# Optimization experiments

Measured on AMD Instinct MI355X. Metric: run time of the kernel, lower is better.

## Reference

```python
import jax, jax.numpy as jnp
import numpy as np

N = 500000   # total nodes in batched graph
B = 8192     # number of graphs
H = 128      # hidden_dim
L = 3        # num_layer -> feature_dim F = H*L = 384
F = H * L
S2S_STEPS = 3
VOCAB = 143


def setup_inputs() -> dict:
    key = jax.random.key(0)
    ks = jax.random.split(key, 12)
    sc = 0.02
    unit_type = jax.random.randint(ks[0], (N,), 0, VOCAB)
    # sorted segment ids covering every graph (contiguous, all B segments non-empty)
    node2graph = (jnp.arange(N) * B) // N
    return {
        'unit_type': unit_type,
        'node2graph': node2graph,
        'embed':    jax.random.normal(ks[1], (VOCAB, H)) * sc,
        'msg_W1':   jax.random.normal(ks[2], (H, 2 * H)) * sc,
        'msg_b1':   jnp.zeros((H,)),
        'msg_W2':   jax.random.normal(ks[3], (H, H)) * sc,
        'msg_b2':   jnp.zeros((H,)),
        'gru_Wih':  jax.random.normal(ks[4], (3 * H, H)) * sc,
        'gru_Whh':  jax.random.normal(ks[5], (3 * H, H)) * sc,
        'gru_bih':  jnp.zeros((3 * H,)),
        'gru_bhh':  jnp.zeros((3 * H,)),
        'lstm_Wih': jax.random.normal(ks[6], (4 * F, 2 * F)) * sc,
        'lstm_Whh': jax.random.normal(ks[7], (4 * F, F)) * sc,
        'lstm_bih': jnp.zeros((4 * F,)),
        'lstm_bhh': jnp.zeros((4 * F,)),
    }


def _gru_step(x, h, Wih, Whh, bih, bhh):
    # single-timestep PyTorch GRU cell; gate order r, z, n
    gi = x @ Wih.T + bih
    gh = h @ Whh.T + bhh
    ir, iz, inn = jnp.split(gi, 3, axis=-1)
    hr, hz, hn = jnp.split(gh, 3, axis=-1)
    r = jax.nn.sigmoid(ir + hr)
    z = jax.nn.sigmoid(iz + hz)
    n = jnp.tanh(inn + r * hn)
    return (1.0 - z) * n + z * h


def _lstm_step(x, h, c, Wih, Whh, bih, bhh):
    # single-timestep PyTorch LSTM cell; gate order i, f, g, o
    g = x @ Wih.T + bih + h @ Whh.T + bhh
    i, f, gc, o = jnp.split(g, 4, axis=-1)
    c = jax.nn.sigmoid(f) * c + jax.nn.sigmoid(i) * jnp.tanh(gc)
    h = jax.nn.sigmoid(o) * jnp.tanh(c)
    return h, c


def reference(unit_type, node2graph, embed, msg_W1, msg_b1, msg_W2, msg_b2,
              gru_Wih, gru_Whh, gru_bih, gru_bhh,
              lstm_Wih, lstm_Whh, lstm_bih, lstm_bhh):
    # --- node update stack ---
    layer_input = embed[unit_type]          # [N, H]
    hx = layer_input                        # GRU hidden state (1 layer)
    hiddens = []
    for _ in range(L):
        x2 = jnp.concatenate([layer_input, layer_input], axis=-1)   # [N, 2H]
        msg = jnp.maximum(x2 @ msg_W1.T + msg_b1, 0.0) @ msg_W2.T + msg_b2
        hx = _gru_step(msg, hx, gru_Wih, gru_Whh, gru_bih, gru_bhh)
        hiddens.append(hx)
        layer_input = hx
    node_feature = jnp.concatenate(hiddens, axis=-1)                # [N, F]

    # --- Set2Set readout ---
    h = jnp.zeros((B, F), dtype=node_feature.dtype)
    c = jnp.zeros((B, F), dtype=node_feature.dtype)
    q_star = jnp.zeros((B, 2 * F), dtype=node_feature.dtype)
    for _ in range(S2S_STEPS):
        h, c = _lstm_step(q_star, h, c, lstm_Wih, lstm_Whh, lstm_bih, lstm_bhh)
        q = h                                                       # [B, F]
        logits = jnp.sum(q[node2graph] * node_feature, axis=-1)     # [N]
        m = jax.ops.segment_max(logits, node2graph, num_segments=B,
                                indices_are_sorted=True)
        e = jnp.exp(logits - m[node2graph])
        z = jax.ops.segment_sum(e, node2graph, num_segments=B,
                                indices_are_sorted=True)
        att = e / z[node2graph]                                     # [N]
        pooled = jax.ops.segment_sum(att[:, None] * node_feature, node2graph,
                                     num_segments=B, indices_are_sorted=True)
        q_star = jnp.concatenate([q, pooled], axis=-1)              # [B, 2F]

    return q_star, node_feature
```

## Files before the change

### kernel.cpp

```cpp
#include <hip/hip_runtime.h>

typedef unsigned short u16;
typedef unsigned int   u32;
typedef u16 bfx8 __attribute__((ext_vector_type(8)));
typedef __bf16 bf16x8 __attribute__((ext_vector_type(8)));
typedef float  f32x4  __attribute__((ext_vector_type(4)));

#define NH  128
#define NF  384
#define K2F 768
#define NG4 1536

__device__ __forceinline__ float bf2f(u16 u){ return __uint_as_float(((u32)u) << 16); }
__device__ __forceinline__ u16 f2bf(float f){
  u32 x = __float_as_uint(f);
  u32 r = x + 0x7fffu + ((x >> 16) & 1u);
  return (u16)(r >> 16);
}
__device__ __forceinline__ float fsig(float x){ return 1.0f / (1.0f + __expf(-x)); }
__device__ __forceinline__ float ftanh(float x){ return 1.0f - 2.0f / (__expf(2.0f * x) + 1.0f); }

struct P {
  const int *unit_type, *n2g;
  const void *embed, *w1, *b1, *w2, *b2, *gwih, *gwhh, *gbih, *gbhh, *lwih, *lwhh, *lbih, *lbhh;
  int *flag, *segS, *segE;
  u16 *W1eb, *W2b, *Wihb, *Whhb;
  float *b1f, *b2f, *bihG, *bhhG;
  float *Wcat;
  float *bsum;
  float *h1v, *c1v;
  float *hbuf, *cbuf, *pooled;
  float *xcat;
  float *gout;
  u16 *nfb;
  int useNfb;
  void *out; long qsz;
  int N, B, embedN;
};

__device__ __forceinline__ float ldin(const void* p, long i, int isbf){
  return isbf ? bf2f(((const u16*)p)[i]) : ((const float*)p)[i];
}

__global__ void k_detect(P p){
  __shared__ int cnt;
  if (threadIdx.x == 0) cnt = 0;
  __syncthreads();
  const u32* w = (const u32*)p.embed;
  const int nw = p.embedN / 2;
  int bad = 0;
  for (int i = threadIdx.x; i < nw; i += blockDim.x){
    u32 v = w[i];
    float fhi = __uint_as_float(v & 0xffff0000u);
    float flo = __uint_as_float(v << 16);
    if (!(fabsf(fhi) < 2.0f)) bad++;
    if (!(fabsf(flo) < 2.0f)) bad++;
  }
  atomicAdd(&cnt, bad);
  __syncthreads();
  if (threadIdx.x == 0) *p.flag = (cnt == 0) ? 1 : 0;
}

__global__ void k_prep(P p){
  long o = (long)blockIdx.x * 256 + threadIdx.x;
  const int isbf = *p.flag;
  if (o < 16384){ long cc = o >> 7, k = o & 127;
    float v = ldin(p.w1, cc*256 + k, isbf) + ldin(p.w1, cc*256 + 128 + k, isbf);
    p.W1eb[o] = f2bf(v); return; } o -= 16384;
  if (o < 16384){ p.W2b[o]  = f2bf(ldin(p.w2, o, isbf));   return; } o -= 16384;
  if (o < 49152){ p.Wihb[o] = f2bf(ldin(p.gwih, o, isbf)); return; } o -= 49152;
  if (o < 49152){ p.Whhb[o] = f2bf(ldin(p.gwhh, o, isbf)); return; } o -= 49152;
  if (o < (long)NG4*K2F){ long j = o / K2F, k = o - j*K2F;
    float v = ldin(p.lwih, o, isbf);
    if (k < NF) v += ldin(p.lwhh, j*NF + k, isbf);
    p.Wcat[o] = v; return; } o -= (long)NG4*K2F;
  if (o < NH){ p.b1f[o] = ldin(p.b1, o, isbf); return; } o -= NH;
  if (o < NH){ p.b2f[o] = ldin(p.b2, o, isbf); return; } o -= NH;
  if (o < NF){ p.bihG[o] = ldin(p.gbih, o, isbf); return; } o -= NF;
  if (o < NF){ p.bhhG[o] = ldin(p.gbhh, o, isbf); return; } o -= NF;
  if (o < NG4){ p.bsum[o] = ldin(p.lbih, o, isbf) + ldin(p.lbhh, o, isbf); return; } o -= NG4;
  if (o < p.B){ p.segS[o] = 0; p.segE[o] = 0; }
}

__global__ void k_segb(P p){
  int i = (int)blockIdx.x * 256 + threadIdx.x;
  if (i >= p.N) return;
  int g = p.n2g[i];
  if (g < 0 || g >= p.B) return;
  if (i == 0        || p.n2g[i-1] != g) p.segS[g] = i;
  if (i == p.N - 1  || p.n2g[i+1] != g) p.segE[g] = i + 1;
}

__device__ __forceinline__ f32x4 MF(bf16x8 a, bf16x8 b, f32x4 c){
  return __builtin_amdgcn_mfma_f32_16x16x32_bf16(a, b, c, 0, 0, 0);
}
__device__ __forceinline__ bf16x8 ldA(const u16* buf, int m0, int k0, int lane){
  const int row = m0 + (lane & 15);
  const int byte = (row*256 + (k0 + (lane>>4)*8)*2) ^ ((row&7)<<4);
  return *(const bf16x8*)((const char*)buf + byte);
}
__device__ __forceinline__ bf16x8 ldB(const u16* __restrict__ W, int n0, int k0, int lane){
  return *(const bf16x8*)(W + (long)(n0 + (lane&15))*NH + k0 + (lane>>4)*8);
}
__device__ __forceinline__ void stLDS(u16* buf, int row, int col, float v){
  const int byte = (row*256 + col*2) ^ ((row&7)<<4);
  *(u16*)((char*)buf + byte) = f2bf(v);
}
__device__ __forceinline__ float ldLDS(const u16* buf, int row, int col){
  const int byte = (row*256 + col*2) ^ ((row&7)<<4);
  return bf2f(*(const u16*)((const char*)buf + byte));
}
__device__ __forceinline__ u16 ldLDSraw(const u16* buf, int row, int col){
  const int byte = (row*256 + col*2) ^ ((row&7)<<4);
  return *(const u16*)((const char*)buf + byte);
}

__global__ __launch_bounds__(256, 3) void k_stageA_mfma(P p){
  __shared__ u16 hA[64*128];
  __shared__ u16 mA[64*128];
  __shared__ u16 gA[64*128];
  const int t = (int)threadIdx.x;
  const int lane = t & 63, w = t >> 6;
  const int node0 = (int)blockIdx.x * 64;
  const int cL = lane & 15;
  const int isbf = *p.flag;

  {
    const int row = t >> 2, seg = t & 3;
    const int node = min(node0 + row, p.N - 1);
    int ut = p.unit_type[node];
    ut = min(max(ut, 0), p.embedN/NH - 1);
    if (isbf){
      const u16* src = (const u16*)p.embed + (long)ut*NH + seg*32;
      #pragma unroll
      for (int i = 0; i < 4; ++i){
        const int col = seg*32 + i*8;
        const int byte = (row*256 + col*2) ^ ((row&7)<<4);
        *(bfx8*)((char*)hA + byte) = *(const bfx8*)(src + i*8);
      }
    } else {
      const float* src = (const float*)p.embed + (long)ut*NH + seg*32;
      #pragma unroll
      for (int i = 0; i < 4; ++i){
        const int col = seg*32 + i*8;
        u16 tmp[8];
        #pragma unroll
        for (int j = 0; j < 8; ++j) tmp[j] = f2bf(src[i*8 + j]);
        const int byte = (row*256 + col*2) ^ ((row&7)<<4);
        *(bfx8*)((char*)hA + byte) = *(const bfx8*)tmp;
      }
    }
  }
  __syncthreads();

  u16*   out16 = (u16*)p.out;
  float* out32 = (float*)p.out;

  #pragma unroll 1
  for (int l = 0; l < 3; ++l){
    {
      f32x4 acc[2][4];
      #pragma unroll
      for (int nt = 0; nt < 2; ++nt){
        const float b = p.b1f[w*32 + nt*16 + cL];
        #pragma unroll
        for (int m = 0; m < 4; ++m) acc[nt][m] = {b,b,b,b};
      }
      for (int k0 = 0; k0 < 128; k0 += 32){
        bf16x8 a[4];
        #pragma unroll
        for (int m = 0; m < 4; ++m) a[m] = ldA(hA, m*16, k0, lane);
        #pragma unroll
        for (int nt = 0; nt < 2; ++nt){
          const bf16x8 b = ldB(p.W1eb, w*32 + nt*16, k0, lane);
          #pragma unroll
          for (int m = 0; m < 4; ++m) acc[nt][m] = MF(a[m], b, acc[nt][m]);
        }
      }
      #pragma unroll
      for (int nt = 0; nt < 2; ++nt)
        #pragma unroll
        for (int m = 0; m < 4; ++m)
          #pragma unroll
          for (int j = 0; j < 4; ++j)
            stLDS(mA, m*16 + (lane>>4)*4 + j, w*32 + nt*16 + cL,
                  fmaxf(acc[nt][m][j], 0.0f));
    }
    __syncthreads();
    {
      f32x4 acc[2][4];
      #pragma unroll
      for (int nt = 0; nt < 2; ++nt){
        const float b = p.b2f[w*32 + nt*16 + cL];
        #pragma unroll
        for (int m = 0; m < 4; ++m) acc[nt][m] = {b,b,b,b};
      }
      for (int k0 = 0; k0 < 128; k0 += 32){
        bf16x8 a[4];
        #pragma unroll
        for (int m = 0; m < 4; ++m) a[m] = ldA(mA, m*16, k0, lane);
        #pragma unroll
        for (int nt = 0; nt < 2; ++nt){
          const bf16x8 b = ldB(p.W2b, w*32 + nt*16, k0, lane);
          #pragma unroll
          for (int m = 0; m < 4; ++m) acc[nt][m] = MF(a[m], b, acc[nt][m]);
        }
      }
      __syncthreads();
      #pragma unroll
      for (int nt = 0; nt < 2; ++nt)
        #pragma unroll
        for (int m = 0; m < 4; ++m)
          #pragma unroll
          for (int j = 0; j < 4; ++j)
            stLDS(gA, m*16 + (lane>>4)*4 + j, w*32 + nt*16 + cL, acc[nt][m][j]);
    }
    __syncthreads();
    f32x4 rr[2][4];
    {
      f32x4 acc[4][4];
      #pragma unroll
      for (int tc = 0; tc < 4; ++tc){
        const int col = (tc < 2 ? 0 : 128) + w*32 + (tc&1)*16 + cL;
        const float b = p.bihG[col] + p.bhhG[col];
        #pragma unroll
        for (int m = 0; m < 4; ++m) acc[tc][m] = {b,b,b,b};
      }
      for (int k0 = 0; k0 < 128; k0 += 32){
        bf16x8 a[4];
        #pragma unroll
        for (int m = 0; m < 4; ++m) a[m] = ldA(gA, m*16, k0, lane);
        #pragma unroll
        for (int tc = 0; tc < 4; ++tc){
          const bf16x8 b = ldB(p.Wihb, (tc < 2 ? 0 : 128) + w*32 + (tc&1)*16, k0, lane);
          #pragma unroll
          for (int m = 0; m < 4; ++m) acc[tc][m] = MF(a[m], b, acc[tc][m]);
        }
      }
      for (int k0 = 0; k0 < 128; k0 += 32){
        bf16x8 a[4];
        #pragma unroll
        for (int m = 0; m < 4; ++m) a[m] = ldA(hA, m*16, k0, lane);
        #pragma unroll
        for (int tc = 0; tc < 4; ++tc){
          const bf16x8 b = ldB(p.Whhb, (tc < 2 ? 0 : 128) + w*32 + (tc&1)*16, k0, lane);
          #pragma unroll
          for (int m = 0; m < 4; ++m) acc[tc][m] = MF(a[m], b, acc[tc][m]);
        }
      }
      #pragma unroll
      for (int nt = 0; nt < 2; ++nt)
        #pragma unroll
        for (int m = 0; m < 4; ++m)
          #pragma unroll
          for (int j = 0; j < 4; ++j){
            rr[nt][m][j] = fsig(acc[nt][m][j]);
            stLDS(mA, m*16 + (lane>>4)*4 + j, w*32 + nt*16 + cL,
                  fsig(acc[nt+2][m][j]));
          }
    }
    {
      f32x4 inn[2][4], hnn[2][4];
      #pragma unroll
      for (int nt = 0; nt < 2; ++nt){
        const int col = 256 + w*32 + nt*16 + cL;
        const float bi = p.bihG[col], bh = p.bhhG[col];
        #pragma unroll
        for (int m = 0; m < 4; ++m){ inn[nt][m] = {bi,bi,bi,bi}; hnn[nt][m] = {bh,bh,bh,bh}; }
      }
      for (int k0 = 0; k0 < 128; k0 += 32){
        bf16x8 a[4];
        #pragma unroll
        for (int m = 0; m < 4; ++m) a[m] = ldA(gA, m*16, k0, lane);
        #pragma unroll
        for (int nt = 0; nt < 2; ++nt){
          const bf16x8 b = ldB(p.Wihb, 256 + w*32 + nt*16, k0, lane);
          #pragma unroll
          for (int m = 0; m < 4; ++m) inn[nt][m] = MF(a[m], b, inn[nt][m]);
        }
      }
      for (int k0 = 0; k0 < 128; k0 += 32){
        bf16x8 a[4];
        #pragma unroll
        for (int m = 0; m < 4; ++m) a[m] = ldA(hA, m*16, k0, lane);
        #pragma unroll
        for (int nt = 0; nt < 2; ++nt){
          const bf16x8 b = ldB(p.Whhb, 256 + w*32 + nt*16, k0, lane);
          #pragma unroll
          for (int m = 0; m < 4; ++m) hnn[nt][m] = MF(a[m], b, hnn[nt][m]);
        }
      }
      #pragma unroll
      for (int nt = 0; nt < 2; ++nt)
        #pragma unroll
        for (int m = 0; m < 4; ++m)
          #pragma unroll
          for (int j = 0; j < 4; ++j){
            const int row = m*16 + (lane>>4)*4 + j;
            const int col = w*32 + nt*16 + cL;
            const float nn = ftanh(fmaf(rr[nt][m][j], hnn[nt][m][j], inn[nt][m][j]));
            const float zv = ldLDS(mA, row, col);
            const float hv = ldLDS(hA, row, col);
            inn[nt][m][j] = fmaf(zv, hv - nn, nn);
          }
      __syncthreads();
      #pragma unroll
      for (int nt = 0; nt < 2; ++nt)
        #pragma unroll
        for (int m = 0; m < 4; ++m)
          #pragma unroll
          for (int j = 0; j < 4; ++j)
            stLDS(hA, m*16 + (lane>>4)*4 + j, w*32 + nt*16 + cL, inn[nt][m][j]);
      __syncthreads();
    }
    {
      const int col = t & 127;
      const int rh  = t >> 7;
      #pragma unroll 4
      for (int rb = 0; rb < 64; rb += 2){
        const int row = rb + rh;
        const int node = node0 + row;
        if (node < p.N){
          const u16 hv16 = ldLDSraw(hA, row, col);
          const long fi = (long)node*NF + l*NH + col;
          if (isbf){
            __builtin_nontemporal_store(hv16, &out16[p.qsz + fi]);
          } else {
            __builtin_nontemporal_store(bf2f(hv16), &out32[p.qsz + fi]);
            if (p.useNfb) __builtin_nontemporal_store(hv16, &p.nfb[fi]);
          }
        }
      }
    }
  }
}

__global__ void k_lstm0(P p){
  const int d = (int)threadIdx.x;
  if (d >= NF) return;
  const float i_ = fsig(p.bsum[d]);
  const float gc = ftanh(p.bsum[2*NF + d]);
  const float o_ = fsig(p.bsum[3*NF + d]);
  const float cn = i_ * gc;
  p.c1v[d] = cn;
  p.h1v[d] = o_ * ftanh(cn);
}

__global__ __launch_bounds__(256) void k_attn(P p, const float* __restrict__ qsrc,
                                              int qstride, int finalstep){
  __shared__ alignas(16) char raw[32 * NF * 4];
  __shared__ float qs[NF];
  __shared__ float att[32];
  __shared__ float sM, sZ, sSc;

  u16*   nb = (u16*)raw;
  float* nfl = (float*)raw;
  const int t = (int)threadIdx.x;
  const int g = (int)blockIdx.x;
  const int isbf = *p.flag;
  const int bftile = isbf | p.useNfb;
  const u16* nbase = isbf ? (const u16*)p.out + p.qsz : p.nfb;
  const float* o32 = (const float*)p.out;

  for (int i = t; i < NF; i += 256) qs[i] = qsrc[(long)g*qstride + i];
  if (t == 0){ sM = -1e30f; sZ = 0.0f; sSc = 1.0f; }
  int n0 = p.segS[g], n1 = p.segE[g];
  n0 = max(n0, 0); n1 = min(n1, p.N);
  float acc0 = 0.f, acc1 = 0.f;
  __syncthreads();

  for (int base = n0; base < n1; base += 32){
    const int cnt = min(32, n1 - base);
    {
      const int i = t >> 3, q8 = t & 7;
      if (i < cnt){
        if (bftile){
          const bfx8* src = (const bfx8*)(nbase + (long)(base + i)*NF + q8*48);
          #pragma unroll
          for (int j8 = 0; j8 < 6; ++j8)
            *(bfx8*)&nb[i*NF + q8*48 + j8*8] = __builtin_nontemporal_load(src + j8);
        } else {
          const f32x4* src = (const f32x4*)(o32 + p.qsz + (long)(base + i)*NF + q8*48);
          #pragma unroll
          for (int j4 = 0; j4 < 12; ++j4)
            *(f32x4*)&nfl[i*NF + q8*48 + j4*4] = __builtin_nontemporal_load(src + j4);
        }
      }
    }
    __syncthreads();
    {
      const int w = t >> 6, lane = t & 63;
      for (int ii = w; ii < cnt; ii += 4){
        float dot = 0.f;
        #pragma unroll
        for (int j = 0; j < 6; ++j){
          const int d = lane + 64*j;
          const float v = bftile ? bf2f(nb[ii*NF + d]) : nfl[ii*NF + d];
          dot = fmaf(v, qs[d], dot);
        }
        #pragma unroll
        for (int off = 32; off; off >>= 1) dot += __shfl_xor(dot, off);
        if (lane == 0) att[ii] = dot;
      }
    }
    __syncthreads();
    if (t < 32){
      const float l = (t < cnt) ? att[t] : -1e30f;
      float m = l;
      #pragma unroll
      for (int off = 16; off; off >>= 1) m = fmaxf(m, __shfl_xor(m, off));
      const float mnew = fmaxf(sM, m);
      const float e = (t < cnt) ? __expf(l - mnew) : 0.f;
      float z = e;
      #pragma unroll
      for (int off = 16; off; off >>= 1) z += __shfl_xor(z, off);
      if (t < cnt) att[t] = e;
      if (t == 0){
        const float sc = __expf(sM - mnew);
        sSc = sc; sZ = sZ * sc + z; sM = mnew;
      }
    }
    __syncthreads();
    {
      const float sc = sSc;
      acc0 *= sc; acc1 *= sc;
      for (int ii = 0; ii < cnt; ++ii){
        const float a = att[ii];
        const float v0 = bftile ? bf2f(nb[ii*NF + t]) : nfl[ii*NF + t];
        acc0 = fmaf(a, v0, acc0);
        if (t < 128){
          const float v1 = bftile ? bf2f(nb[ii*NF + 256 + t]) : nfl[ii*NF + 256 + t];
          acc1 = fmaf(a, v1, acc1);
        }
      }
    }
    __syncthreads();
  }

  const float invZ = (sZ != 0.0f) ? 1.0f / sZ : 0.0f;
  const float p0 = acc0 * invZ, p1 = acc1 * invZ;
  p.pooled[(long)g*NF + t] = p0;
  if (t < 128) p.pooled[(long)g*NF + 256 + t] = p1;
  if (finalstep){
    const long rb = (long)g * K2F;
    if (isbf){
      u16* o = (u16*)p.out;
      o[rb + t] = f2bf(qs[t]);
      if (t < 128) o[rb + 256 + t] = f2bf(qs[256 + t]);
      o[rb + NF + t] = f2bf(p0);
      if (t < 128) o[rb + NF + 256 + t] = f2bf(p1);
    } else {
      float* o = (float*)p.out;
      o[rb + t] = qs[t];
      if (t < 128) o[rb + 256 + t] = qs[256 + t];
      o[rb + NF + t] = p0;
      if (t < 128) o[rb + NF + 256 + t] = p1;
    }
  }
}

__global__ void k_xcat(P p, const float* __restrict__ hsrc, int hstride){
  const int d2 = (int)blockIdx.x * 256 + threadIdx.x;
  const int g  = (int)blockIdx.y;
  if (d2 >= K2F) return;
  const float v = (d2 < NF) ? hsrc[(long)g*hstride + d2]
                            : p.pooled[(long)g*NF + d2 - NF];
  p.xcat[(long)g*K2F + d2] = v;
}

__global__ __launch_bounds__(256) void k_gemm(P p){
  __shared__ alignas(16) float aT[32][128];
  __shared__ alignas(16) float wT[32][128];
  const int t = (int)threadIdx.x;
  const int tx = t & 15, ty = t >> 4;
  const int row0 = (int)blockIdx.x * 128, col0 = (int)blockIdx.y * 128;
  const int M = p.B;
  float acc[8][8];
  #pragma unroll
  for (int i = 0; i < 8; ++i)
    #pragma unroll
    for (int j = 0; j < 8; ++j) acc[i][j] = 0.f;

  const int r = t >> 1, ks = (t & 1) * 16;
  for (int kc = 0; kc < K2F; kc += 32){
    {
      const int gr = row0 + r;
      float v[16];
      if (gr < M){
        const float* src = p.xcat + (long)gr*K2F + kc + ks;
        *(float4*)&v[0]  = *(const float4*)(src);
        *(float4*)&v[4]  = *(const float4*)(src + 4);
        *(float4*)&v[8]  = *(const float4*)(src + 8);
        *(float4*)&v[12] = *(const float4*)(src + 12);
      } else {
        #pragma unroll
        for (int j = 0; j < 16; ++j) v[j] = 0.f;
      }
      #pragma unroll
      for (int j = 0; j < 16; ++j) aT[ks+j][r] = v[j];
      const float* wsrc = p.Wcat + (long)(col0 + r)*K2F + kc + ks;
      *(float4*)&v[0]  = *(const float4*)(wsrc);
      *(float4*)&v[4]  = *(const float4*)(wsrc + 4);
      *(float4*)&v[8]  = *(const float4*)(wsrc + 8);
      *(float4*)&v[12] = *(const float4*)(wsrc + 12);
      #pragma unroll
      for (int j = 0; j < 16; ++j) wT[ks+j][r] = v[j];
    }
    __syncthreads();
    #pragma unroll 2
    for (int k = 0; k < 32; ++k){
      float a[8], wv[8];
      *(float4*)&a[0]  = *(const float4*)&aT[k][ty*8];
      *(float4*)&a[4]  = *(const float4*)&aT[k][ty*8 + 4];
      *(float4*)&wv[0] = *(const float4*)&wT[k][tx*8];
      *(float4*)&wv[4] = *(const float4*)&wT[k][tx*8 + 4];
      #pragma unroll
      for (int i = 0; i < 8; ++i)
        #pragma unroll
        for (int j = 0; j < 8; ++j) acc[i][j] = fmaf(a[i], wv[j], acc[i][j]);
    }
    __syncthreads();
  }
  float bs[8];
  #pragma unroll
  for (int j = 0; j < 8; ++j) bs[j] = p.bsum[col0 + tx*8 + j];
  #pragma unroll
  for (int i = 0; i < 8; ++i){
    const int gr = row0 + ty*8 + i;
    if (gr < M){
      float* crow = p.gout + (long)gr*NG4 + col0 + tx*8;
      float o[8];
      #pragma unroll
      for (int j = 0; j < 8; ++j) o[j] = acc[i][j] + bs[j];
      *(float4*)&crow[0] = *(const float4*)&o[0];
      *(float4*)&crow[4] = *(const float4*)&o[4];
    }
  }
}

__global__ void k_gates(P p, const float* __restrict__ csrc, int cstride){
  const long idx = (long)blockIdx.x * 256 + threadIdx.x;
  if (idx >= (long)p.B * NF) return;
  const int g = (int)(idx / NF), d = (int)(idx - (long)g*NF);
  const float* gr = p.gout + (long)g*NG4;
  const float i_ = fsig(gr[d]);
  const float f_ = fsig(gr[NF + d]);
  const float gc = ftanh(gr[2*NF + d]);
  const float o_ = fsig(gr[3*NF + d]);
  const float cp = csrc[(long)g*cstride + d];
  const float cn = fmaf(f_, cp, i_ * gc);
  p.cbuf[(long)g*NF + d] = cn;
  p.hbuf[(long)g*NF + d] = o_ * ftanh(cn);
}

extern "C" void kernel_launch(void* const* d_in, const int* in_sizes, int n_in,
                              void* d_out, int out_size, void* d_ws, size_t ws_size,
                              hipStream_t stream){
  P p{};
  p.unit_type = (const int*)d_in[0];
  p.n2g  = (const int*)d_in[1];
  p.embed = d_in[2];  p.w1 = d_in[3];  p.b1 = d_in[4];  p.w2 = d_in[5];  p.b2 = d_in[6];
  p.gwih = d_in[7];  p.gwhh = d_in[8]; p.gbih = d_in[9]; p.gbhh = d_in[10];
  p.lwih = d_in[11]; p.lwhh = d_in[12]; p.lbih = d_in[13]; p.lbhh = d_in[14];

  const int N = in_sizes[0];
  const int B = (int)(((long)out_size - (long)N*NF) / K2F);
  p.N = N; p.B = B; p.embedN = in_sizes[2];
  p.out = d_out; p.qsz = (long)B * K2F;

  char* w = (char*)d_ws;
  size_t used = 0;
  auto alloc = [&](size_t bytes) -> char* {
    char* r = w + used;
    used += (bytes + 255) & ~(size_t)255;
    return r;
  };
  p.flag  = (int*)alloc(4);
  p.segS  = (int*)alloc((size_t)B*4);
  p.segE  = (int*)alloc((size_t)B*4);
  p.W1eb  = (u16*)  alloc(16384*2);
  p.W2b   = (u16*)  alloc(16384*2);
  p.Wihb  = (u16*)  alloc(49152*2);
  p.Whhb  = (u16*)  alloc(49152*2);
  p.b1f   = (float*)alloc(NH*4);
  p.b2f   = (float*)alloc(NH*4);
  p.bihG  = (float*)alloc(NF*4);
  p.bhhG  = (float*)alloc(NF*4);
  p.Wcat  = (float*)alloc((size_t)NG4*K2F*4);
  p.bsum  = (float*)alloc(NG4*4);
  p.h1v   = (float*)alloc(NF*4);
  p.c1v   = (float*)alloc(NF*4);
  p.hbuf  = (float*)alloc((size_t)B*NF*4);
  p.cbuf  = (float*)alloc((size_t)B*NF*4);
  p.pooled= (float*)alloc((size_t)B*NF*4);
  p.xcat  = (float*)alloc((size_t)B*K2F*4);
  p.gout  = (float*)alloc((size_t)B*NG4*4);
  if (used > ws_size){
    (void)hipMemsetAsync(d_out, 0, (size_t)out_size * 2, stream);
    return;
  }
  const size_t nfbBytes = (size_t)N * NF * 2;
  if (used + nfbBytes + 256 <= ws_size){
    p.nfb = (u16*)alloc(nfbBytes);
    p.useNfb = 1;
  } else {
    p.nfb = (u16*)p.flag;
    p.useNfb = 0;
  }

  const long prepTot = 16384 + 16384 + 49152 + 49152
                     + (long)NG4*K2F + NH + NH + NF + NF + NG4 + B;

  k_detect<<<1, 256, 0, stream>>>(p);
  k_prep  <<<(int)((prepTot + 255)/256), 256, 0, stream>>>(p);
  k_segb  <<<(N + 255)/256, 256, 0, stream>>>(p);
  k_stageA_mfma<<<(N + 63)/64, 256, 0, stream>>>(p);
  k_lstm0 <<<1, NF, 0, stream>>>(p);

  const int gemmGx = (B + 127)/128;
  k_attn <<<B, 256, 0, stream>>>(p, p.h1v, 0, 0);
  k_xcat <<<dim3(3, B), 256, 0, stream>>>(p, p.h1v, 0);
  k_gemm <<<dim3(gemmGx, NG4/128), 256, 0, stream>>>(p);
  k_gates<<<(int)(((long)B*NF + 255)/256), 256, 0, stream>>>(p, p.c1v, 0);
  k_attn <<<B, 256, 0, stream>>>(p, p.hbuf, NF, 0);
  k_xcat <<<dim3(3, B), 256, 0, stream>>>(p, p.hbuf, NF);
  k_gemm <<<dim3(gemmGx, NG4/128), 256, 0, stream>>>(p);
  k_gates<<<(int)(((long)B*NF + 255)/256), 256, 0, stream>>>(p, p.cbuf, NF);
  k_attn <<<B, 256, 0, stream>>>(p, p.hbuf, NF, 1);
}
```

Baseline: 2.265 ms.

## Defer node-feature stores to one vectorized write of all three layers

```diff
diff --git a/kernel.cpp b/kernel.cpp
--- a/kernel.cpp
+++ b/kernel.cpp
@@ -106,13 +106,17 @@
   const int byte = (row*256 + col*2) ^ ((row&7)<<4);
   *(u16*)((char*)buf + byte) = f2bf(v);
 }
+__device__ __forceinline__ void stLDSu(u16* buf, int row, int col, u16 v){
+  const int byte = (row*256 + col*2) ^ ((row&7)<<4);
+  *(u16*)((char*)buf + byte) = v;
+}
 __device__ __forceinline__ float ldLDS(const u16* buf, int row, int col){
   const int byte = (row*256 + col*2) ^ ((row&7)<<4);
   return bf2f(*(const u16*)((const char*)buf + byte));
 }
-__device__ __forceinline__ u16 ldLDSraw(const u16* buf, int row, int col){
-  const int byte = (row*256 + col*2) ^ ((row&7)<<4);
-  return *(const u16*)((const char*)buf + byte);
+__device__ __forceinline__ bfx8 ldLDS8(const u16* buf, int row, int col8){
+  const int byte = (row*256 + col8*2) ^ ((row&7)<<4);
+  return *(const bfx8*)((const char*)buf + byte);
 }
 
 __global__ __launch_bounds__(256, 3) void k_stageA_mfma(P p){
@@ -125,6 +129,8 @@
   const int cL = lane & 15;
   const int isbf = *p.flag;
 
+  u16 st[2][2][4][4];
+
   {
     const int row = t >> 2, seg = t & 3;
     const int node = min(node0 + row, p.N - 1);
@@ -309,25 +315,59 @@
         #pragma unroll
         for (int m = 0; m < 4; ++m)
           #pragma unroll
-          for (int j = 0; j < 4; ++j)
-            stLDS(hA, m*16 + (lane>>4)*4 + j, w*32 + nt*16 + cL, inn[nt][m][j]);
+          for (int j = 0; j < 4; ++j){
+            const u16 hv16 = f2bf(inn[nt][m][j]);
+            stLDSu(hA, m*16 + (lane>>4)*4 + j, w*32 + nt*16 + cL, hv16);
+            if (l == 0) st[0][nt][m][j] = hv16;
+            else if (l == 1) st[1][nt][m][j] = hv16;
+          }
       __syncthreads();
     }
-    {
-      const int col = t & 127;
-      const int rh  = t >> 7;
-      #pragma unroll 4
-      for (int rb = 0; rb < 64; rb += 2){
-        const int row = rb + rh;
-        const int node = node0 + row;
-        if (node < p.N){
-          const u16 hv16 = ldLDSraw(hA, row, col);
-          const long fi = (long)node*NF + l*NH + col;
-          if (isbf){
-            __builtin_nontemporal_store(hv16, &out16[p.qsz + fi]);
-          } else {
-            __builtin_nontemporal_store(bf2f(hv16), &out32[p.qsz + fi]);
-            if (p.useNfb) __builtin_nontemporal_store(hv16, &p.nfb[fi]);
+  }
+
+  #pragma unroll
+  for (int nt = 0; nt < 2; ++nt)
+    #pragma unroll
+    for (int m = 0; m < 4; ++m)
+      #pragma unroll
+      for (int j = 0; j < 4; ++j){
+        const int row = m*16 + (lane>>4)*4 + j;
+        const int col = w*32 + nt*16 + cL;
+        stLDSu(mA, row, col, st[0][nt][m][j]);
+        stLDSu(gA, row, col, st[1][nt][m][j]);
+      }
+  __syncthreads();
+
+  {
+    const int r0 = t >> 4;
+    const int c8 = (t & 15) * 8;
+    #pragma unroll
+    for (int r4 = 0; r4 < 4; ++r4){
+      const int row = r0 + r4*16;
+      const int node = node0 + row;
+      if (node < p.N){
+        const bfx8 v0 = ldLDS8(mA, row, c8);
+        const bfx8 v1 = ldLDS8(gA, row, c8);
+        const bfx8 v2 = ldLDS8(hA, row, c8);
+        const long base = (long)node*NF;
+        if (isbf){
+          __builtin_nontemporal_store(v0, (bfx8*)(out16 + p.qsz + base + c8));
+          __builtin_nontemporal_store(v1, (bfx8*)(out16 + p.qsz + base + NH + c8));
+          __builtin_nontemporal_store(v2, (bfx8*)(out16 + p.qsz + base + 2*NH + c8));
+        } else {
+          #pragma unroll
+          for (int lyr = 0; lyr < 3; ++lyr){
+            const bfx8 v = lyr == 0 ? v0 : (lyr == 1 ? v1 : v2);
+            f32x4 lo, hi;
+            #pragma unroll
+            for (int j = 0; j < 4; ++j){ lo[j] = bf2f(v[j]); hi[j] = bf2f(v[j+4]); }
+            __builtin_nontemporal_store(lo, (f32x4*)(out32 + p.qsz + base + lyr*NH + c8));
+            __builtin_nontemporal_store(hi, (f32x4*)(out32 + p.qsz + base + lyr*NH + c8 + 4));
+          }
+          if (p.useNfb){
+            __builtin_nontemporal_store(v0, (bfx8*)(p.nfb + base + c8));
+            __builtin_nontemporal_store(v1, (bfx8*)(p.nfb + base + NH + c8));
+            __builtin_nontemporal_store(v2, (bfx8*)(p.nfb + base + 2*NH + c8));
           }
         }
       }
```

Result: slower. 2.373 ms (+4.7%).

## Move LSTM gate GEMM to bf16 MFMA and persist stage-A tiles

Applied to the files above, without the earlier changes.

```diff
diff --git a/kernel.cpp b/kernel.cpp
--- a/kernel.cpp
+++ b/kernel.cpp
@@ -24,13 +24,14 @@
   const int *unit_type, *n2g;
   const void *embed, *w1, *b1, *w2, *b2, *gwih, *gwhh, *gbih, *gbhh, *lwih, *lwhh, *lbih, *lbhh;
   int *flag, *segS, *segE;
+  u16 *embedB;
   u16 *W1eb, *W2b, *Wihb, *Whhb;
   float *b1f, *b2f, *bihG, *bhhG;
-  float *Wcat;
+  u16 *WcatB;
   float *bsum;
   float *h1v, *c1v;
   float *hbuf, *cbuf, *pooled;
-  float *xcat;
+  u16 *xcatB;
   float *gout;
   u16 *nfb;
   int useNfb;
@@ -64,6 +65,7 @@
 __global__ void k_prep(P p){
   long o = (long)blockIdx.x * 256 + threadIdx.x;
   const int isbf = *p.flag;
+  if (o < p.embedN){ p.embedB[o] = f2bf(ldin(p.embed, o, isbf)); return; } o -= p.embedN;
   if (o < 16384){ long cc = o >> 7, k = o & 127;
     float v = ldin(p.w1, cc*256 + k, isbf) + ldin(p.w1, cc*256 + 128 + k, isbf);
     p.W1eb[o] = f2bf(v); return; } o -= 16384;
@@ -73,7 +75,7 @@
   if (o < (long)NG4*K2F){ long j = o / K2F, k = o - j*K2F;
     float v = ldin(p.lwih, o, isbf);
     if (k < NF) v += ldin(p.lwhh, j*NF + k, isbf);
-    p.Wcat[o] = v; return; } o -= (long)NG4*K2F;
+    p.WcatB[o] = f2bf(v); return; } o -= (long)NG4*K2F;
   if (o < NH){ p.b1f[o] = ldin(p.b1, o, isbf); return; } o -= NH;
   if (o < NH){ p.b2f[o] = ldin(p.b2, o, isbf); return; } o -= NH;
   if (o < NF){ p.bihG[o] = ldin(p.gbih, o, isbf); return; } o -= NF;
@@ -102,6 +104,10 @@
 __device__ __forceinline__ bf16x8 ldB(const u16* __restrict__ W, int n0, int k0, int lane){
   return *(const bf16x8*)(W + (long)(n0 + (lane&15))*NH + k0 + (lane>>4)*8);
 }
+__device__ __forceinline__ bf16x8 ldBs(const u16* __restrict__ W, long stride,
+                                       int n0, int k0, int lane){
+  return *(const bf16x8*)(W + (long)(n0 + (lane&15))*stride + k0 + (lane>>4)*8);
+}
 __device__ __forceinline__ void stLDS(u16* buf, int row, int col, float v){
   const int byte = (row*256 + col*2) ^ ((row&7)<<4);
   *(u16*)((char*)buf + byte) = f2bf(v);
@@ -121,213 +127,205 @@
   __shared__ u16 gA[64*128];
   const int t = (int)threadIdx.x;
   const int lane = t & 63, w = t >> 6;
-  const int node0 = (int)blockIdx.x * 64;
   const int cL = lane & 15;
   const int isbf = *p.flag;
-
-  {
-    const int row = t >> 2, seg = t & 3;
-    const int node = min(node0 + row, p.N - 1);
-    int ut = p.unit_type[node];
-    ut = min(max(ut, 0), p.embedN/NH - 1);
-    if (isbf){
-      const u16* src = (const u16*)p.embed + (long)ut*NH + seg*32;
+  const int nTiles = (p.N + 63) >> 6;
+
+  u16*   out16 = (u16*)p.out;
+  float* out32 = (float*)p.out;
+
+  for (int tile = (int)blockIdx.x; tile < nTiles; tile += (int)gridDim.x){
+    const int node0 = tile * 64;
+    __syncthreads();
+
+    {
+      const int row = t >> 2, seg = t & 3;
+      const int node = min(node0 + row, p.N - 1);
+      int ut = p.unit_type[node];
+      ut = min(max(ut, 0), p.embedN/NH - 1);
+      const u16* src = p.embedB + (long)ut*NH + seg*32;
       #pragma unroll
       for (int i = 0; i < 4; ++i){
         const int col = seg*32 + i*8;
         const int byte = (row*256 + col*2) ^ ((row&7)<<4);
         *(bfx8*)((char*)hA + byte) = *(const bfx8*)(src + i*8);
       }
-    } else {
-      const float* src = (const float*)p.embed + (long)ut*NH + seg*32;
-      #pragma unroll
-      for (int i = 0; i < 4; ++i){
-        const int col = seg*32 + i*8;
-        u16 tmp[8];
-        #pragma unroll
-        for (int j = 0; j < 8; ++j) tmp[j] = f2bf(src[i*8 + j]);
-        const int byte = (row*256 + col*2) ^ ((row&7)<<4);
-        *(bfx8*)((char*)hA + byte) = *(const bfx8*)tmp;
-      }
-    }
-  }
-  __syncthreads();
-
-  u16*   out16 = (u16*)p.out;
-  float* out32 = (float*)p.out;
-
-  #pragma unroll 1
-  for (int l = 0; l < 3; ++l){
-    {
-      f32x4 acc[2][4];
-      #pragma unroll
-      for (int nt = 0; nt < 2; ++nt){
-        const float b = p.b1f[w*32 + nt*16 + cL];
-        #pragma unroll
-        for (int m = 0; m < 4; ++m) acc[nt][m] = {b,b,b,b};
-      }
-      for (int k0 = 0; k0 < 128; k0 += 32){
-        bf16x8 a[4];
-        #pragma unroll
-        for (int m = 0; m < 4; ++m) a[m] = ldA(hA, m*16, k0, lane);
+    }
+    __syncthreads();
+
+    #pragma unroll 1
+    for (int l = 0; l < 3; ++l){
+      {
+        f32x4 acc[2][4];
         #pragma unroll
         for (int nt = 0; nt < 2; ++nt){
-          const bf16x8 b = ldB(p.W1eb, w*32 + nt*16, k0, lane);
-          #pragma unroll
-          for (int m = 0; m < 4; ++m) acc[nt][m] = MF(a[m], b, acc[nt][m]);
-        }
-      }
-      #pragma unroll
-      for (int nt = 0; nt < 2; ++nt)
-        #pragma unroll
-        for (int m = 0; m < 4; ++m)
-          #pragma unroll
-          for (int j = 0; j < 4; ++j)
-            stLDS(mA, m*16 + (lane>>4)*4 + j, w*32 + nt*16 + cL,
-                  fmaxf(acc[nt][m][j], 0.0f));
-    }
-    __syncthreads();
-    {
-      f32x4 acc[2][4];
-      #pragma unroll
-      for (int nt = 0; nt < 2; ++nt){
-        const float b = p.b2f[w*32 + nt*16 + cL];
-        #pragma unroll
-        for (int m = 0; m < 4; ++m) acc[nt][m] = {b,b,b,b};
-      }
-      for (int k0 = 0; k0 < 128; k0 += 32){
-        bf16x8 a[4];
-        #pragma unroll
-        for (int m = 0; m < 4; ++m) a[m] = ldA(mA, m*16, k0, lane);
+          const float b = p.b1f[w*32 + nt*16 + cL];
+          #pragma unroll
+          for (int m = 0; m < 4; ++m) acc[nt][m] = {b,b,b,b};
+        }
+        for (int k0 = 0; k0 < 128; k0 += 32){
+          bf16x8 a[4];
+          #pragma unroll
+          for (int m = 0; m < 4; ++m) a[m] = ldA(hA, m*16, k0, lane);
+          #pragma unroll
+          for (int nt = 0; nt < 2; ++nt){
+            const bf16x8 b = ldB(p.W1eb, w*32 + nt*16, k0, lane);
+            #pragma unroll
+            for (int m = 0; m < 4; ++m) acc[nt][m] = MF(a[m], b, acc[nt][m]);
+          }
+        }
+        #pragma unroll
+        for (int nt = 0; nt < 2; ++nt)
+          #pragma unroll
+          for (int m = 0; m < 4; ++m)
+            #pragma unroll
+            for (int j = 0; j < 4; ++j)
+              stLDS(mA, m*16 + (lane>>4)*4 + j, w*32 + nt*16 + cL,
+                    fmaxf(acc[nt][m][j], 0.0f));
+      }
+      __syncthreads();
+      {
+        f32x4 acc[2][4];
         #pragma unroll
         for (int nt = 0; nt < 2; ++nt){
-          const bf16x8 b = ldB(p.W2b, w*32 + nt*16, k0, lane);
-          #pragma unroll
-          for (int m = 0; m < 4; ++m) acc[nt][m] = MF(a[m], b, acc[nt][m]);
-        }
+          const float b = p.b2f[w*32 + nt*16 + cL];
+          #pragma unroll
+          for (int m = 0; m < 4; ++m) acc[nt][m] = {b,b,b,b};
+        }
+        for (int k0 = 0; k0 < 128; k0 += 32){
+          bf16x8 a[4];
+          #pragma unroll
+          for (int m = 0; m < 4; ++m) a[m] = ldA(mA, m*16, k0, lane);
+          #pragma unroll
+          for (int nt = 0; nt < 2; ++nt){
+            const bf16x8 b = ldB(p.W2b, w*32 + nt*16, k0, lane);
+            #pragma unroll
+            for (int m = 0; m < 4; ++m) acc[nt][m] = MF(a[m], b, acc[nt][m]);
+          }
+        }
+        __syncthreads();
+        #pragma unroll
+        for (int nt = 0; nt < 2; ++nt)
+          #pragma unroll
+          for (int m = 0; m < 4; ++m)
+            #pragma unroll
+            for (int j = 0; j < 4; ++j)
+              stLDS(gA, m*16 + (lane>>4)*4 + j, w*32 + nt*16 + cL, acc[nt][m][j]);
       }
       __syncthreads();
-      #pragma unroll
-      for (int nt = 0; nt < 2; ++nt)
-        #pragma unroll
-        for (int m = 0; m < 4; ++m)
-          #pragma unroll
-          for (int j = 0; j < 4; ++j)
-            stLDS(gA, m*16 + (lane>>4)*4 + j, w*32 + nt*16 + cL, acc[nt][m][j]);
-    }
-    __syncthreads();
-    f32x4 rr[2][4];
-    {
-      f32x4 acc[4][4];
-      #pragma unroll
-      for (int tc = 0; tc < 4; ++tc){
-        const int col = (tc < 2 ? 0 : 128) + w*32 + (tc&1)*16 + cL;
-        const float b = p.bihG[col] + p.bhhG[col];
-        #pragma unroll
-        for (int m = 0; m < 4; ++m) acc[tc][m] = {b,b,b,b};
-      }
-      for (int k0 = 0; k0 < 128; k0 += 32){
-        bf16x8 a[4];
-        #pragma unroll
-        for (int m = 0; m < 4; ++m) a[m] = ldA(gA, m*16, k0, lane);
+      f32x4 rr[2][4];
+      {
+        f32x4 acc[4][4];
         #pragma unroll
         for (int tc = 0; tc < 4; ++tc){
-          const bf16x8 b = ldB(p.Wihb, (tc < 2 ? 0 : 128) + w*32 + (tc&1)*16, k0, lane);
-          #pragma unroll
-          for (int m = 0; m < 4; ++m) acc[tc][m] = MF(a[m], b, acc[tc][m]);
-        }
-      }
-      for (int k0 = 0; k0 < 128; k0 += 32){
-        bf16x8 a[4];
-        #pragma unroll
-        for (int m = 0; m < 4; ++m) a[m] = ldA(hA, m*16, k0, lane);
-        #pragma unroll
-        for (int tc = 0; tc < 4; ++tc){
-          const bf16x8 b = ldB(p.Whhb, (tc < 2 ? 0 : 128) + w*32 + (tc&1)*16, k0, lane);
-          #pragma unroll
-          for (int m = 0; m < 4; ++m) acc[tc][m] = MF(a[m], b, acc[tc][m]);
-        }
-      }
-      #pragma unroll
-      for (int nt = 0; nt < 2; ++nt)
-        #pragma unroll
-        for (int m = 0; m < 4; ++m)
-          #pragma unroll
-          for (int j = 0; j < 4; ++j){
-            rr[nt][m][j] = fsig(acc[nt][m][j]);
-            stLDS(mA, m*16 + (lane>>4)*4 + j, w*32 + nt*16 + cL,
-                  fsig(acc[nt+2][m][j]));
+          const int col = (tc < 2 ? 0 : 128) + w*32 + (tc&1)*16 + cL;
+          const float b = p.bihG[col] + p.bhhG[col];
+          #pragma unroll
+          for (int m = 0; m < 4; ++m) acc[tc][m] = {b,b,b,b};
+        }
+        for (int k0 = 0; k0 < 128; k0 += 32){
+          bf16x8 a[4];
+          #pragma unroll
+          for (int m = 0; m < 4; ++m) a[m] = ldA(gA, m*16, k0, lane);
+          #pragma unroll
+          for (int tc = 0; tc < 4; ++tc){
+            const bf16x8 b = ldB(p.Wihb, (tc < 2 ? 0 : 128) + w*32 + (tc&1)*16, k0, lane);
+            #pragma unroll
+            for (int m = 0; m < 4; ++m) acc[tc][m] = MF(a[m], b, acc[tc][m]);
           }
-    }
-    {
-      f32x4 inn[2][4], hnn[2][4];
-      #pragma unroll
-      for (int nt = 0; nt < 2; ++nt){
-        const int col = 256 + w*32 + nt*16 + cL;
-        const float bi = p.bihG[col], bh = p.bhhG[col];
-        #pragma unroll
-        for (int m = 0; m < 4; ++m){ inn[nt][m] = {bi,bi,bi,bi}; hnn[nt][m] = {bh,bh,bh,bh}; }
-      }
-      for (int k0 = 0; k0 < 128; k0 += 32){
-        bf16x8 a[4];
-        #pragma unroll
-        for (int m = 0; m < 4; ++m) a[m] = ldA(gA, m*16, k0, lane);
+        }
+        for (int k0 = 0; k0 < 128; k0 += 32){
+          bf16x8 a[4];
+          #pragma unroll
+          for (int m = 0; m < 4; ++m) a[m] = ldA(hA, m*16, k0, lane);
+          #pragma unroll
+          for (int tc = 0; tc < 4; ++tc){
+            const bf16x8 b = ldB(p.Whhb, (tc < 2 ? 0 : 128) + w*32 + (tc&1)*16, k0, lane);
+            #pragma unroll
+            for (int m = 0; m < 4; ++m) acc[tc][m] = MF(a[m], b, acc[tc][m]);
+          }
+        }
+        #pragma unroll
+        for (int nt = 0; nt < 2; ++nt)
+          #pragma unroll
+          for (int m = 0; m < 4; ++m)
+            #pragma unroll
+            for (int j = 0; j < 4; ++j){
+              rr[nt][m][j] = fsig(acc[nt][m][j]);
+              stLDS(mA, m*16 + (lane>>4)*4 + j, w*32 + nt*16 + cL,
+                    fsig(acc[nt+2][m][j]));
+            }
+      }
+      {
+        f32x4 inn[2][4], hnn[2][4];
         #pragma unroll
         for (int nt = 0; nt < 2; ++nt){
-          const bf16x8 b = ldB(p.Wihb, 256 + w*32 + nt*16, k0, lane);
-          #pragma unroll
-          for (int m = 0; m < 4; ++m) inn[nt][m] = MF(a[m], b, inn[nt][m]);
-        }
-      }
-      for (int k0 = 0; k0 < 128; k0 += 32){
-        bf16x8 a[4];
-        #pragma unroll
-        for (int m = 0; m < 4; ++m) a[m] = ldA(hA, m*16, k0, lane);
-        #pragma unroll
-        for (int nt = 0; nt < 2; ++nt){
-          const bf16x8 b = ldB(p.Whhb, 256 + w*32 + nt*16, k0, lane);
-          #pragma unroll
-          for (int m = 0; m < 4; ++m) hnn[nt][m] = MF(a[m], b, hnn[nt][m]);
-        }
-      }
-      #pragma unroll
-      for (int nt = 0; nt < 2; ++nt)
-        #pragma unroll
-        for (int m = 0; m < 4; ++m)
-          #pragma unroll
-          for (int j = 0; j < 4; ++j){
-            const int row = m*16 + (lane>>4)*4 + j;
-            const int col = w*32 + nt*16 + cL;
-            const float nn = ftanh(fmaf(rr[nt][m][j], hnn[nt][m][j], inn[nt][m][j]));
-            const float zv = ldLDS(mA, row, col);
-            const float hv = ldLDS(hA, row, col);
-            inn[nt][m][j] = fmaf(zv, hv - nn, nn);
+          const int col = 256 + w*32 + nt*16 + cL;
+          const float bi = p.bihG[col], bh = p.bhhG[col];
+          #pragma unroll
+          for (int m = 0; m < 4; ++m){ inn[nt][m] = {bi,bi,bi,bi}; hnn[nt][m] = {bh,bh,bh,bh}; }
+        }
+        for (int k0 = 0; k0 < 128; k0 += 32){
+          bf16x8 a[4];
+          #pragma unroll
+          for (int m = 0; m < 4; ++m) a[m] = ldA(gA, m*16, k0, lane);
+          #pragma unroll
+          for (int nt = 0; nt < 2; ++nt){
+            const bf16x8 b = ldB(p.Wihb, 256 + w*32 + nt*16, k0, lane);
+            #pragma unroll
+            for (int m = 0; m < 4; ++m) inn[nt][m] = MF(a[m], b, inn[nt][m]);
           }
-      __syncthreads();
-      #pragma unroll
-      for (int nt = 0; nt < 2; ++nt)
-        #pragma unroll
-        for (int m = 0; m < 4; ++m)
-          #pragma unroll
-          for (int j = 0; j < 4; ++j)
-            stLDS(hA, m*16 + (lane>>4)*4 + j, w*32 + nt*16 + cL, inn[nt][m][j]);
-      __syncthreads();
-    }
-    {
-      const int col = t & 127;
-      const int rh  = t >> 7;
-      #pragma unroll 4
-      for (int rb = 0; rb < 64; rb += 2){
-        const int row = rb + rh;
-        const int node = node0 + row;
-        if (node < p.N){
-          const u16 hv16 = ldLDSraw(hA, row, col);
-          const long fi = (long)node*NF + l*NH + col;
-          if (isbf){
-            __builtin_nontemporal_store(hv16, &out16[p.qsz + fi]);
-          } else {
-            __builtin_nontemporal_store(bf2f(hv16), &out32[p.qsz + fi]);
-            if (p.useNfb) __builtin_nontemporal_store(hv16, &p.nfb[fi]);
+        }
+        for (int k0 = 0; k0 < 128; k0 += 32){
+          bf16x8 a[4];
+          #pragma unroll
+          for (int m = 0; m < 4; ++m) a[m] = ldA(hA, m*16, k0, lane);
+          #pragma unroll
+          for (int nt = 0; nt < 2; ++nt){
+            const bf16x8 b = ldB(p.Whhb, 256 + w*32 + nt*16, k0, lane);
+            #pragma unroll
+            for (int m = 0; m < 4; ++m) hnn[nt][m] = MF(a[m], b, hnn[nt][m]);
+          }
+        }
+        #pragma unroll
+        for (int nt = 0; nt < 2; ++nt)
+          #pragma unroll
+          for (int m = 0; m < 4; ++m)
+            #pragma unroll
+            for (int j = 0; j < 4; ++j){
+              const int row = m*16 + (lane>>4)*4 + j;
+              const int col = w*32 + nt*16 + cL;
+              const float nn = ftanh(fmaf(rr[nt][m][j], hnn[nt][m][j], inn[nt][m][j]));
+              const float zv = ldLDS(mA, row, col);
+              const float hv = ldLDS(hA, row, col);
+              inn[nt][m][j] = fmaf(zv, hv - nn, nn);
+            }
+        __syncthreads();
+        #pragma unroll
+        for (int nt = 0; nt < 2; ++nt)
+          #pragma unroll
+          for (int m = 0; m < 4; ++m)
+            #pragma unroll
+            for (int j = 0; j < 4; ++j)
+              stLDS(hA, m*16 + (lane>>4)*4 + j, w*32 + nt*16 + cL, inn[nt][m][j]);
+        __syncthreads();
+      }
+      {
+        const int col = t & 127;
+        const int rh  = t >> 7;
+        #pragma unroll 4
+        for (int rb = 0; rb < 64; rb += 2){
+          const int row = rb + rh;
+          const int node = node0 + row;
+          if (node < p.N){
+            const u16 hv16 = ldLDSraw(hA, row, col);
+            const long fi = (long)node*NF + l*NH + col;
+            if (isbf){
+              __builtin_nontemporal_store(hv16, &out16[p.qsz + fi]);
+            } else {
+              __builtin_nontemporal_store(bf2f(hv16), &out32[p.qsz + fi]);
+              if (p.useNfb) __builtin_nontemporal_store(hv16, &p.nfb[fi]);
+            }
           }
         }
       }
@@ -465,76 +463,60 @@
   if (d2 >= K2F) return;
   const float v = (d2 < NF) ? hsrc[(long)g*hstride + d2]
                             : p.pooled[(long)g*NF + d2 - NF];
-  p.xcat[(long)g*K2F + d2] = v;
-}
-
-__global__ __launch_bounds__(256) void k_gemm(P p){
-  __shared__ alignas(16) float aT[32][128];
-  __shared__ alignas(16) float wT[32][128];
+  p.xcatB[(long)g*K2F + d2] = f2bf(v);
+}
+
+__global__ __launch_bounds__(256, 4) void k_gemm_mfma(P p){
+  __shared__ u16 aT[64*128];
   const int t = (int)threadIdx.x;
-  const int tx = t & 15, ty = t >> 4;
-  const int row0 = (int)blockIdx.x * 128, col0 = (int)blockIdx.y * 128;
-  const int M = p.B;
-  float acc[8][8];
+  const int lane = t & 63, w = t >> 6, cL = lane & 15;
+  const int row0 = (int)blockIdx.x * 64, col0 = (int)blockIdx.y * 128;
+
+  f32x4 acc[2][4];
   #pragma unroll
-  for (int i = 0; i < 8; ++i)
+  for (int nt = 0; nt < 2; ++nt)
     #pragma unroll
-    for (int j = 0; j < 8; ++j) acc[i][j] = 0.f;
-
-  const int r = t >> 1, ks = (t & 1) * 16;
-  for (int kc = 0; kc < K2F; kc += 32){
+    for (int m = 0; m < 4; ++m) acc[nt][m] = {0.f,0.f,0.f,0.f};
+
+  for (int kc = 0; kc < K2F; kc += 128){
+    __syncthreads();
     {
-      const int gr = row0 + r;
-      float v[16];
-      if (gr < M){
-        const float* src = p.xcat + (long)gr*K2F + kc + ks;
-        *(float4*)&v[0]  = *(const float4*)(src);
-        *(float4*)&v[4]  = *(const float4*)(src + 4);
-        *(float4*)&v[8]  = *(const float4*)(src + 8);
-        *(float4*)&v[12] = *(const float4*)(src + 12);
-      } else {
-        #pragma unroll
-        for (int j = 0; j < 16; ++j) v[j] = 0.f;
-      }
+      const int row = t >> 2, seg = t & 3;
+      const int gr = row0 + row;
+      const u16* src = p.xcatB + (long)gr*K2F + kc + seg*32;
       #pragma unroll
-      for (int j = 0; j < 16; ++j) aT[ks+j][r] = v[j];
-      const float* wsrc = p.Wcat + (long)(col0 + r)*K2F + kc + ks;
-      *(float4*)&v[0]  = *(const float4*)(wsrc);
-      *(float4*)&v[4]  = *(const float4*)(wsrc + 4);
-      *(float4*)&v[8]  = *(const float4*)(wsrc + 8);
-      *(float4*)&v[12] = *(const float4*)(wsrc + 12);
+      for (int i = 0; i < 4; ++i){
+        const int col = seg*32 + i*8;
+        const int byte = (row*256 + col*2) ^ ((row&7)<<4);
+        bfx8 v = {0,0,0,0,0,0,0,0};
+        if (gr < p.B) v = *(const bfx8*)(src + i*8);
+        *(bfx8*)((char*)aT + byte) = v;
+      }
+    }
+    __syncthreads();
+    for (int k0 = 0; k0 < 128; k0 += 32){
+      bf16x8 a[4];
       #pragma unroll
-      for (int j = 0; j < 16; ++j) wT[ks+j][r] = v[j];
-    }
-    __syncthreads();
-    #pragma unroll 2
-    for (int k = 0; k < 32; ++k){
-      float a[8], wv[8];
-      *(float4*)&a[0]  = *(const float4*)&aT[k][ty*8];
-      *(float4*)&a[4]  = *(const float4*)&aT[k][ty*8 + 4];
-      *(float4*)&wv[0] = *(const float4*)&wT[k][tx*8];
-      *(float4*)&wv[4] = *(const float4*)&wT[k][tx*8 + 4];
+      for (int m = 0; m < 4; ++m) a[m] = ldA(aT, m*16, k0, lane);
       #pragma unroll
-      for (int i = 0; i < 8; ++i)
-        #pragma unroll
-        for (int j = 0; j < 8; ++j) acc[i][j] = fmaf(a[i], wv[j], acc[i][j]);
-    }
-    __syncthreads();
-  }
-  float bs[8];
+      for (int nt = 0; nt < 2; ++nt){
+        const bf16x8 b = ldBs(p.WcatB, K2F, col0 + w*32 + nt*16, kc + k0, lane);
+        #pragma unroll
+        for (int m = 0; m < 4; ++m) acc[nt][m] = MF(a[m], b, acc[nt][m]);
+      }
+    }
+  }
   #pragma unroll
-  for (int j = 0; j < 8; ++j) bs[j] = p.bsum[col0 + tx*8 + j];
-  #pragma unroll
-  for (int i = 0; i < 8; ++i){
-    const int gr = row0 + ty*8 + i;
-    if (gr < M){
-      float* crow = p.gout + (long)gr*NG4 + col0 + tx*8;
-      float o[8];
+  for (int nt = 0; nt < 2; ++nt){
+    const int col = col0 + w*32 + nt*16 + cL;
+    const float bs = p.bsum[col];
+    #pragma unroll
+    for (int m = 0; m < 4; ++m)
       #pragma unroll
-      for (int j = 0; j < 8; ++j) o[j] = acc[i][j] + bs[j];
-      *(float4*)&crow[0] = *(const float4*)&o[0];
-      *(float4*)&crow[4] = *(const float4*)&o[4];
-    }
+      for (int j = 0; j < 4; ++j){
+        const int row = row0 + m*16 + (lane>>4)*4 + j;
+        if (row < p.B) p.gout[(long)row*NG4 + col] = acc[nt][m][j] + bs;
+      }
   }
 }
 
@@ -578,6 +560,7 @@
   p.flag  = (int*)alloc(4);
   p.segS  = (int*)alloc((size_t)B*4);
   p.segE  = (int*)alloc((size_t)B*4);
+  p.embedB= (u16*)  alloc((size_t)p.embedN*2);
   p.W1eb  = (u16*)  alloc(16384*2);
   p.W2b   = (u16*)  alloc(16384*2);
   p.Wihb  = (u16*)  alloc(49152*2);
@@ -586,14 +569,14 @@
   p.b2f   = (float*)alloc(NH*4);
   p.bihG  = (float*)alloc(NF*4);
   p.bhhG  = (float*)alloc(NF*4);
-  p.Wcat  = (float*)alloc((size_t)NG4*K2F*4);
+  p.WcatB = (u16*)  alloc((size_t)NG4*K2F*2);
   p.bsum  = (float*)alloc(NG4*4);
   p.h1v   = (float*)alloc(NF*4);
   p.c1v   = (float*)alloc(NF*4);
   p.hbuf  = (float*)alloc((size_t)B*NF*4);
   p.cbuf  = (float*)alloc((size_t)B*NF*4);
   p.pooled= (float*)alloc((size_t)B*NF*4);
-  p.xcat  = (float*)alloc((size_t)B*K2F*4);
+  p.xcatB = (u16*)  alloc((size_t)B*K2F*2);
   p.gout  = (float*)alloc((size_t)B*NG4*4);
   if (used > ws_size){
     (void)hipMemsetAsync(d_out, 0, (size_t)out_size * 2, stream);
@@ -608,23 +591,24 @@
     p.useNfb = 0;
   }
 
-  const long prepTot = 16384 + 16384 + 49152 + 49152
+  const long prepTot = (long)p.embedN + 16384 + 16384 + 49152 + 49152
                      + (long)NG4*K2F + NH + NH + NF + NF + NG4 + B;
 
   k_detect<<<1, 256, 0, stream>>>(p);
   k_prep  <<<(int)((prepTot + 255)/256), 256, 0, stream>>>(p);
   k_segb  <<<(N + 255)/256, 256, 0, stream>>>(p);
-  k_stageA_mfma<<<(N + 63)/64, 256, 0, stream>>>(p);
+  const int saGrid = min((N + 63)/64, 2048);
+  k_stageA_mfma<<<saGrid, 256, 0, stream>>>(p);
   k_lstm0 <<<1, NF, 0, stream>>>(p);
 
-  const int gemmGx = (B + 127)/128;
+  const dim3 gemmG((B + 63)/64, NG4/128);
   k_attn <<<B, 256, 0, stream>>>(p, p.h1v, 0, 0);
   k_xcat <<<dim3(3, B), 256, 0, stream>>>(p, p.h1v, 0);
-  k_gemm <<<dim3(gemmGx, NG4/128), 256, 0, stream>>>(p);
+  k_gemm_mfma<<<gemmG, 256, 0, stream>>>(p);
   k_gates<<<(int)(((long)B*NF + 255)/256), 256, 0, stream>>>(p, p.c1v, 0);
   k_attn <<<B, 256, 0, stream>>>(p, p.hbuf, NF, 0);
   k_xcat <<<dim3(3, B), 256, 0, stream>>>(p, p.hbuf, NF);
-  k_gemm <<<dim3(gemmGx, NG4/128), 256, 0, stream>>>(p);
+  k_gemm_mfma<<<gemmG, 256, 0, stream>>>(p);
   k_gates<<<(int)(((long)B*NF + 255)/256), 256, 0, stream>>>(p, p.cbuf, NF);
   k_attn <<<B, 256, 0, stream>>>(p, p.hbuf, NF, 1);
 }
```

Result: faster. 2.054 ms (-9.3%).
